# Optimization experiments

Measured on AMD Instinct MI355X. Metric: run time of the kernel, lower is better.

The kernel has to match this reference:

```python
import jax, jax.numpy as jnp
import numpy as np
from jax import lax

B, C, H, W = 8, 64, 128, 128
KS = 3          # kernel size
K = KS * KS     # kernel field = 9
PAD = 1


def conv2d(x, w, b):
    # x: [B,Cin,H,W], w: [Cout,Cin,kh,kw], 'same' 3x3 conv
    y = lax.conv_general_dilated(x, w, window_strides=(1, 1),
                                 padding=((PAD, PAD), (PAD, PAD)),
                                 dimension_numbers=('NCHW', 'OIHW', 'NCHW'))
    return y + b[None, :, None, None]


def modulated_deform_conv(x, offset, mask, weight, bias):
    # x:[B,C,H,W], offset:[B,2K,H,W] (dy,dx per tap), mask:[B,K,H,W]
    Bs, Cin, Hin, Win = x.shape
    off = offset.reshape(Bs, K, 2, Hin, Win)
    ky, kx = jnp.meshgrid(jnp.arange(KS), jnp.arange(KS), indexing='ij')
    ky = ky.reshape(K).astype(x.dtype)   # kernel tap row offsets 0..2
    kx = kx.reshape(K).astype(x.dtype)
    # sampling positions p = p0 + p_k + offset (stride=1, pad=1)
    py = (jnp.arange(Hin, dtype=x.dtype)[None, None, :, None] - PAD
          + ky[None, :, None, None] + off[:, :, 0])            # [B,K,H,W]
    px = (jnp.arange(Win, dtype=x.dtype)[None, None, None, :] - PAD
          + kx[None, :, None, None] + off[:, :, 1])            # [B,K,H,W]

    y0 = jnp.floor(py); x0 = jnp.floor(px)
    ly = py - y0; lx = px - x0                                  # frac parts
    y0i = y0.astype(jnp.int32); x0i = x0.astype(jnp.int32)

    x_flat = x.reshape(Bs, Cin, Hin * Win)

    def gather(iy, ix):
        valid = ((iy >= 0) & (iy < Hin) & (ix >= 0) & (ix < Win))
        flat = (jnp.clip(iy, 0, Hin - 1) * Win + jnp.clip(ix, 0, Win - 1))
        g = jax.vmap(lambda xb, ib: xb[:, ib])(x_flat, flat.reshape(Bs, -1))
        g = g.reshape(Bs, Cin, K, Hin, Win)
        return g * valid[:, None].astype(x.dtype)

    w00 = ((1 - ly) * (1 - lx))[:, None]  # [B,1,K,H,W]
    w01 = ((1 - ly) * lx)[:, None]
    w10 = (ly * (1 - lx))[:, None]
    w11 = (ly * lx)[:, None]

    val = (w00 * gather(y0i, x0i) + w01 * gather(y0i, x0i + 1)
           + w10 * gather(y0i + 1, x0i) + w11 * gather(y0i + 1, x0i + 1))
    val = val * mask[:, None]                                   # modulation
    out = jnp.einsum('ock,bckhw->bohw', weight.reshape(weight.shape[0], Cin, K), val)
    return out + bias[None, :, None, None]


def setup_inputs() -> dict:
    key = jax.random.key(0)
    ks = jax.random.split(key, 7)
    s = 0.05
    return {
        'x': jax.random.normal(ks[0], (B, C, H, W), jnp.float32),
        'w_om': jax.random.normal(ks[1], (3 * K, C, KS, KS), jnp.float32) * s,
        'b_om': jax.random.normal(ks[2], (3 * K,), jnp.float32) * s,
        'w_dc': jax.random.normal(ks[3], (C, C, KS, KS), jnp.float32) * s,
        'b_dc': jax.random.normal(ks[4], (C,), jnp.float32) * s,
        'w_c': jax.random.normal(ks[5], (C, C, KS, KS), jnp.float32) * s,
        'b_c': jax.random.normal(ks[6], (C,), jnp.float32) * s,
    }


def reference(x, w_om, b_om, w_dc, b_dc, w_c, b_c):
    om = conv2d(x, w_om, b_om)                       # [B,3K,H,W]
    offset, mask_raw = om[:, :2 * K], om[:, 2 * K:]
    mask = 2.0 * jax.nn.sigmoid(mask_raw)
    out = modulated_deform_conv(x, offset, mask, w_dc, b_dc)
    act = jnp.where(out > 0, out, 0.2 * out)         # LeakyReLU(0.2)
    return conv2d(act, w_c, b_c) + x
```

## Files before the change

kernel.cpp:

```cpp
#include <hip/hip_runtime.h>
#include <math.h>

#define Bn 8
#define Cn 64
#define Hn 128
#define Wn 128
#define HWn (Hn * Wn)

#define WOM_OFF 0
#define WDC_OFF 18432
#define WC_OFF 55296

typedef __attribute__((ext_vector_type(8))) short short8;
typedef __attribute__((ext_vector_type(4))) float floatx4;

__device__ __forceinline__ float bf2f(short s) {
  return __uint_as_float(((unsigned)(unsigned short)s) << 16);
}
__device__ __forceinline__ short f2bf(float f) {
  unsigned u = __float_as_uint(f);
  u += 0x7fff + ((u >> 16) & 1);
  return (short)(u >> 16);
}

__global__ __launch_bounds__(256) void k_prep_w(
    const float* __restrict__ w_om, const float* __restrict__ w_dc,
    const float* __restrict__ w_c, short* __restrict__ wt) {
  int idx = blockIdx.x * 256 + threadIdx.x;
  if (idx >= 92160) return;
  float v;
  if (idx < WDC_OFF) {
    int e = idx;
    int elem = e & 7, lane = (e >> 3) & 63, mt = (e >> 9) & 1, t = e >> 10;
    int kk = t % 9, cc = t / 9;
    int row = mt * 16 + (lane & 15);
    int cin = cc * 32 + (lane >> 4) * 8 + elem;
    v = (row < 27) ? w_om[(row * 64 + cin) * 9 + kk] : 0.f;
  } else {
    int e = (idx < WC_OFF) ? idx - WDC_OFF : idx - WC_OFF;
    const float* src = (idx < WC_OFF) ? w_dc : w_c;
    int elem = e & 7, lane = (e >> 3) & 63, mt = (e >> 9) & 3, t = e >> 11;
    int kk = t % 9, cc = t / 9;
    int row = mt * 16 + (lane & 15);
    int cin = cc * 32 + (lane >> 4) * 8 + elem;
    v = src[(row * 64 + cin) * 9 + kk];
  }
  wt[idx] = f2bf(v);
}

__global__ __launch_bounds__(256) void k_prep_x(const float* __restrict__ x,
                                                short* __restrict__ xT) {
  __shared__ float tile[64][129];
  const int bid = blockIdx.x;
  const int b = bid & 7, h = bid >> 3;
  const int tid = threadIdx.x;
  const float* xb = x + (size_t)b * 64 * HWn + h * Wn;
  for (int i = tid; i < 8192; i += 256) {
    int c = i >> 7, w = i & 127;
    tile[c][w] = xb[c * HWn + w];
  }
  __syncthreads();
  short* dst = xT + ((size_t)(b * Hn + h) * Wn) * 64;
  for (int i = tid; i < 2048; i += 256) {
    int w = i >> 4, c4 = (i & 15) * 4;
    short4 o;
    o.x = f2bf(tile[c4 + 0][w]);
    o.y = f2bf(tile[c4 + 1][w]);
    o.z = f2bf(tile[c4 + 2][w]);
    o.w = f2bf(tile[c4 + 3][w]);
    *(short4*)(dst + (size_t)w * 64 + c4) = o;
  }
}

__global__ __launch_bounds__(512, 4) void k_omdef(
    const short* __restrict__ xT, const short* __restrict__ wt,
    const float* __restrict__ b_om, const float* __restrict__ b_dc,
    short* __restrict__ actT) {
  __shared__ float som[27 * 132];

  const int bid = blockIdx.x;
  const int b = bid & 7;
  const int h = bid >> 3;
  const int tid = threadIdx.x;
  const int wave = tid >> 6, lane = tid & 63, quad = lane >> 4, lr = lane & 15;
  const short* xb = xT + (size_t)b * HWn * 64;
  const int pxl = wave * 16 + lr;

  floatx4 zf = {0.f, 0.f, 0.f, 0.f};
  const short8 zz = (short8){0, 0, 0, 0, 0, 0, 0, 0};

  floatx4 aco[2] = {zf, zf};
#pragma unroll 3
  for (int kk = 0; kk < 9; ++kk) {
    int ky = kk / 3, kx = kk - ky * 3;
    int gy = h + ky - 1, gx = pxl + kx - 1;
    bool ok = ((unsigned)gy < (unsigned)Hn) && ((unsigned)gx < (unsigned)Wn);
    int gyc = min(max(gy, 0), Hn - 1), gxc = min(max(gx, 0), Wn - 1);
    const short* rec = xb + (size_t)(gyc * Wn + gxc) * 64 + quad * 8;
#pragma unroll
    for (int cc = 0; cc < 2; ++cc) {
      short8 bf = *(const short8*)(rec + cc * 32);
      if (!ok) bf = zz;
      short8 a0 = *(const short8*)(wt + WOM_OFF +
                                   ((cc * 9 + kk) * 2 + 0) * 512 + lane * 8);
      short8 a1 = *(const short8*)(wt + WOM_OFF +
                                   ((cc * 9 + kk) * 2 + 1) * 512 + lane * 8);
      aco[0] = __builtin_amdgcn_mfma_f32_16x16x32_bf16(a0, bf, aco[0], 0, 0, 0);
      aco[1] = __builtin_amdgcn_mfma_f32_16x16x32_bf16(a1, bf, aco[1], 0, 0, 0);
    }
  }
#pragma unroll
  for (int mt = 0; mt < 2; ++mt) {
#pragma unroll
    for (int rr = 0; rr < 4; ++rr) {
      int co = mt * 16 + quad * 4 + rr;
      if (co < 27) {
        float v = aco[mt][rr] + b_om[co];
        if (co >= 18) v = 2.f / (1.f + expf(-v));
        som[co * 132 + pxl] = v;
      }
    }
  }
  asm volatile("s_waitcnt lgkmcnt(0)" ::: "memory");

  floatx4 acc[4] = {zf, zf, zf, zf};
  const short* wdc = wt + WDC_OFF;
  const int cq = quad * 8;
#pragma unroll 3
  for (int kk = 0; kk < 9; ++kk) {
    float offy = som[(2 * kk) * 132 + pxl];
    float offx = som[(2 * kk + 1) * 132 + pxl];
    float m = som[(18 + kk) * 132 + pxl];
    float py = (float)(h - 1 + (kk / 3)) + offy;
    float px_ = (float)(pxl - 1 + (kk % 3)) + offx;
    float fy = floorf(py), fx = floorf(px_);
    float ly = py - fy, lx = px_ - fx;
    int iy0 = (int)fy, ix0 = (int)fx;
    int iy1 = iy0 + 1, ix1 = ix0 + 1;
    bool vy0 = ((unsigned)iy0 < (unsigned)Hn);
    bool vy1 = ((unsigned)iy1 < (unsigned)Hn);
    bool vx0 = ((unsigned)ix0 < (unsigned)Wn);
    bool vx1 = ((unsigned)ix1 < (unsigned)Wn);
    unsigned cy0 = (unsigned)min(max(iy0, 0), Hn - 1);
    unsigned cy1 = (unsigned)min(max(iy1, 0), Hn - 1);
    unsigned cx0 = (unsigned)min(max(ix0, 0), Wn - 1);
    unsigned cx1 = (unsigned)min(max(ix1, 0), Wn - 1);
    unsigned d0 = cy0 * Wn + cx0, d1 = cy0 * Wn + cx1;
    unsigned d2 = cy1 * Wn + cx0, d3 = cy1 * Wn + cx1;
    float u0 = (vy0 && vx0) ? (1.f - ly) * (1.f - lx) * m : 0.f;
    float u1 = (vy0 && vx1) ? (1.f - ly) * lx * m : 0.f;
    float u2 = (vy1 && vx0) ? ly * (1.f - lx) * m : 0.f;
    float u3 = (vy1 && vx1) ? ly * lx * m : 0.f;

    short8 q0 = *(const short8*)(xb + (size_t)d0 * 64 + cq);
    short8 q1 = *(const short8*)(xb + (size_t)d1 * 64 + cq);
    short8 q2 = *(const short8*)(xb + (size_t)d2 * 64 + cq);
    short8 q3 = *(const short8*)(xb + (size_t)d3 * 64 + cq);
    short8 r0 = *(const short8*)(xb + (size_t)d0 * 64 + 32 + cq);
    short8 r1 = *(const short8*)(xb + (size_t)d1 * 64 + 32 + cq);
    short8 r2 = *(const short8*)(xb + (size_t)d2 * 64 + 32 + cq);
    short8 r3 = *(const short8*)(xb + (size_t)d3 * 64 + 32 + cq);

    short8 bf0, bf1;
#pragma unroll
    for (int e = 0; e < 8; ++e) {
      float f = u0 * bf2f(q0[e]) + u1 * bf2f(q1[e]) + u2 * bf2f(q2[e]) +
                u3 * bf2f(q3[e]);
      bf0[e] = f2bf(f);
    }
#pragma unroll
    for (int e = 0; e < 8; ++e) {
      float f = u0 * bf2f(r0[e]) + u1 * bf2f(r1[e]) + u2 * bf2f(r2[e]) +
                u3 * bf2f(r3[e]);
      bf1[e] = f2bf(f);
    }

#pragma unroll
    for (int mt = 0; mt < 4; ++mt) {
      short8 a0 = *(const short8*)(wdc + ((0 * 9 + kk) * 4 + mt) * 512 +
                                   lane * 8);
      acc[mt] = __builtin_amdgcn_mfma_f32_16x16x32_bf16(a0, bf0, acc[mt], 0, 0, 0);
    }
#pragma unroll
    for (int mt = 0; mt < 4; ++mt) {
      short8 a1 = *(const short8*)(wdc + ((1 * 9 + kk) * 4 + mt) * 512 +
                                   lane * 8);
      acc[mt] = __builtin_amdgcn_mfma_f32_16x16x32_bf16(a1, bf1, acc[mt], 0, 0, 0);
    }
  }

  short* ab = actT + ((size_t)(b * Hn + h) * Wn) * 64;
#pragma unroll
  for (int mt = 0; mt < 4; ++mt) {
    int c0 = mt * 16 + quad * 4;
    short4 o;
    float v;
    v = acc[mt][0] + b_dc[c0 + 0]; o.x = f2bf(v > 0.f ? v : 0.2f * v);
    v = acc[mt][1] + b_dc[c0 + 1]; o.y = f2bf(v > 0.f ? v : 0.2f * v);
    v = acc[mt][2] + b_dc[c0 + 2]; o.z = f2bf(v > 0.f ? v : 0.2f * v);
    v = acc[mt][3] + b_dc[c0 + 3]; o.w = f2bf(v > 0.f ? v : 0.2f * v);
    *(short4*)(ab + (size_t)pxl * 64 + c0) = o;
  }
}

__global__ __launch_bounds__(512, 4) void k_conv_out(
    const short* __restrict__ actT, const short* __restrict__ wt,
    const float* __restrict__ b_c, const float* __restrict__ x,
    float* __restrict__ out) {
  __shared__ __attribute__((aligned(16))) short rows[24576];

  const int bid = blockIdx.x;
  const int b = bid & 7;
  const int h = bid >> 3;
  const int tid = threadIdx.x;
  const int wave = tid >> 6, lane = tid & 63, quad = lane >> 4, lr = lane & 15;
  const short* ab = actT + (size_t)b * HWn * 64;
  const int pxl = wave * 16 + lr;

  floatx4 zf = {0.f, 0.f, 0.f, 0.f};
  const short8 zz = (short8){0, 0, 0, 0, 0, 0, 0, 0};
  floatx4 acc[4] = {zf, zf, zf, zf};
  short8* rows8 = (short8*)rows;

  {
    const short8* ar8 = (const short8*)ab;
    for (int i = tid; i < 3072; i += 512) {
      int rr = i >> 10, c = i & 1023;
      int px = c >> 3, sl = c & 7;
      int gy = min(max(h - 1 + rr, 0), Hn - 1);
      short8 v = ar8[(size_t)(gy * Wn + px) * 8 + sl];
      rows8[(rr << 10) + (px << 3) + (sl ^ (px & 7))] = v;
    }
  }
  __syncthreads();

#pragma unroll
  for (int cc = 0; cc < 2; ++cc) {
#pragma unroll
    for (int kk = 0; kk < 9; ++kk) {
      int ky = kk / 3, kx = kk - ky * 3;
      int gy = h + ky - 1, gxx = pxl + kx - 1;
      bool ok = ((unsigned)gy < (unsigned)Hn) && ((unsigned)gxx < (unsigned)Wn);
      int gxc = min(max(gxx, 0), Wn - 1);
      short8 bf = rows8[(ky << 10) + (gxc << 3) + ((cc * 4 + quad) ^ (gxc & 7))];
      if (!ok) bf = zz;
#pragma unroll
      for (int mt = 0; mt < 4; ++mt) {
        short8 am = *(const short8*)(wt + WC_OFF + cc * 18432 +
                                     (kk * 4 + mt) * 512 + lane * 8);
        acc[mt] = __builtin_amdgcn_mfma_f32_16x16x32_bf16(am, bf, acc[mt], 0, 0, 0);
      }
    }
  }
  __syncthreads();

  float* ot = (float*)rows;
#pragma unroll
  for (int mt = 0; mt < 4; ++mt) {
#pragma unroll
    for (int rr = 0; rr < 4; ++rr) {
      ot[(mt * 16 + quad * 4 + rr) * 132 + pxl] = acc[mt][rr];
    }
  }
  __syncthreads();

  const int row = tid >> 3, seg = tid & 7;
  const float bias = b_c[row];
  const size_t gbase = ((size_t)(b * 64 + row) * Hn + h) * Wn + seg * 16;
  const float* xr = x + gbase;
  float* op = out + gbase;
#pragma unroll
  for (int j = 0; j < 4; ++j) {
    floatx4 t = *(const floatx4*)&ot[row * 132 + seg * 16 + j * 4];
    floatx4 xv = *(const floatx4*)&xr[j * 4];
    t = t + xv;
    t[0] += bias; t[1] += bias; t[2] += bias; t[3] += bias;
    *(floatx4*)&op[j * 4] = t;
  }
}

extern "C" void kernel_launch(void* const* d_in, const int* in_sizes, int n_in,
                              void* d_out, int out_size, void* d_ws,
                              size_t ws_size, hipStream_t stream) {
  const float* x = (const float*)d_in[0];
  const float* w_om = (const float*)d_in[1];
  const float* b_om = (const float*)d_in[2];
  const float* w_dc = (const float*)d_in[3];
  const float* b_dc = (const float*)d_in[4];
  const float* w_c = (const float*)d_in[5];
  const float* b_c = (const float*)d_in[6];
  float* out = (float*)d_out;

  short* xT = (short*)d_ws;
  short* actT = xT + (size_t)Bn * HWn * 64;
  short* wt = actT + (size_t)Bn * HWn * 64;

  k_prep_w<<<dim3(360), 256, 0, stream>>>(w_om, w_dc, w_c, wt);
  k_prep_x<<<dim3(1024), 256, 0, stream>>>(x, xT);
  k_omdef<<<dim3(1024), 512, 0, stream>>>(xT, wt, b_om, b_dc, actT);
  k_conv_out<<<dim3(1024), 512, 0, stream>>>(actT, wt, b_c, x, out);
}
```

Baseline: 235.4 us.

## Stage five input rows in swizzled LDS for offset conv and deformable gather

```diff
diff --git a/kernel.cpp b/kernel.cpp
--- a/kernel.cpp
+++ b/kernel.cpp
@@ -72,10 +72,11 @@
   }
 }
 
-__global__ __launch_bounds__(512, 4) void k_omdef(
+__global__ __launch_bounds__(512, 2) void k_omdef(
     const short* __restrict__ xT, const short* __restrict__ wt,
     const float* __restrict__ b_om, const float* __restrict__ b_dc,
     short* __restrict__ actT) {
+  __shared__ __attribute__((aligned(16))) short rows[40960];
   __shared__ float som[27 * 132];
 
   const int bid = blockIdx.x;
@@ -88,6 +89,19 @@
 
   floatx4 zf = {0.f, 0.f, 0.f, 0.f};
   const short8 zz = (short8){0, 0, 0, 0, 0, 0, 0, 0};
+  short8* rows8 = (short8*)rows;
+
+  {
+    const short8* xr8 = (const short8*)xb;
+    for (int i = tid; i < 5120; i += 512) {
+      int rr = i >> 10, c = i & 1023;
+      int px = c >> 3, sl = c & 7;
+      int gy = min(max(h - 2 + rr, 0), Hn - 1);
+      short8 v = xr8[(size_t)(gy * Wn + px) * 8 + sl];
+      rows8[(rr << 10) + (px << 3) + (sl ^ (px & 7))] = v;
+    }
+  }
+  __syncthreads();
 
   floatx4 aco[2] = {zf, zf};
 #pragma unroll 3
@@ -95,11 +109,11 @@
     int ky = kk / 3, kx = kk - ky * 3;
     int gy = h + ky - 1, gx = pxl + kx - 1;
     bool ok = ((unsigned)gy < (unsigned)Hn) && ((unsigned)gx < (unsigned)Wn);
-    int gyc = min(max(gy, 0), Hn - 1), gxc = min(max(gx, 0), Wn - 1);
-    const short* rec = xb + (size_t)(gyc * Wn + gxc) * 64 + quad * 8;
+    int gxc = min(max(gx, 0), Wn - 1);
 #pragma unroll
     for (int cc = 0; cc < 2; ++cc) {
-      short8 bf = *(const short8*)(rec + cc * 32);
+      short8 bf =
+          rows8[((ky + 1) << 10) + (gxc << 3) + ((cc * 4 + quad) ^ (gxc & 7))];
       if (!ok) bf = zz;
       short8 a0 = *(const short8*)(wt + WOM_OFF +
                                    ((cc * 9 + kk) * 2 + 0) * 512 + lane * 8);
@@ -141,25 +155,40 @@
     bool vy1 = ((unsigned)iy1 < (unsigned)Hn);
     bool vx0 = ((unsigned)ix0 < (unsigned)Wn);
     bool vx1 = ((unsigned)ix1 < (unsigned)Wn);
-    unsigned cy0 = (unsigned)min(max(iy0, 0), Hn - 1);
-    unsigned cy1 = (unsigned)min(max(iy1, 0), Hn - 1);
-    unsigned cx0 = (unsigned)min(max(ix0, 0), Wn - 1);
-    unsigned cx1 = (unsigned)min(max(ix1, 0), Wn - 1);
-    unsigned d0 = cy0 * Wn + cx0, d1 = cy0 * Wn + cx1;
-    unsigned d2 = cy1 * Wn + cx0, d3 = cy1 * Wn + cx1;
+    int cy0 = min(max(iy0, 0), Hn - 1);
+    int cy1 = min(max(iy1, 0), Hn - 1);
+    int cx0 = min(max(ix0, 0), Wn - 1);
+    int cx1 = min(max(ix1, 0), Wn - 1);
     float u0 = (vy0 && vx0) ? (1.f - ly) * (1.f - lx) * m : 0.f;
     float u1 = (vy0 && vx1) ? (1.f - ly) * lx * m : 0.f;
     float u2 = (vy1 && vx0) ? ly * (1.f - lx) * m : 0.f;
     float u3 = (vy1 && vx1) ? ly * lx * m : 0.f;
 
-    short8 q0 = *(const short8*)(xb + (size_t)d0 * 64 + cq);
-    short8 q1 = *(const short8*)(xb + (size_t)d1 * 64 + cq);
-    short8 q2 = *(const short8*)(xb + (size_t)d2 * 64 + cq);
-    short8 q3 = *(const short8*)(xb + (size_t)d3 * 64 + cq);
-    short8 r0 = *(const short8*)(xb + (size_t)d0 * 64 + 32 + cq);
-    short8 r1 = *(const short8*)(xb + (size_t)d1 * 64 + 32 + cq);
-    short8 r2 = *(const short8*)(xb + (size_t)d2 * 64 + 32 + cq);
-    short8 r3 = *(const short8*)(xb + (size_t)d3 * 64 + 32 + cq);
+    short8 q0, q1, q2, q3, r0, r1, r2, r3;
+    bool inb = (offy >= -1.0f) && (offy < 1.0f);
+    if (__all((int)inb)) {
+      int j0 = cy0 - h + 2, j1 = cy1 - h + 2;
+      int s0q = (cq >> 3), s1q = 4 + (cq >> 3);
+      q0 = rows8[(j0 << 10) + (cx0 << 3) + (s0q ^ (cx0 & 7))];
+      q1 = rows8[(j0 << 10) + (cx1 << 3) + (s0q ^ (cx1 & 7))];
+      q2 = rows8[(j1 << 10) + (cx0 << 3) + (s0q ^ (cx0 & 7))];
+      q3 = rows8[(j1 << 10) + (cx1 << 3) + (s0q ^ (cx1 & 7))];
+      r0 = rows8[(j0 << 10) + (cx0 << 3) + (s1q ^ (cx0 & 7))];
+      r1 = rows8[(j0 << 10) + (cx1 << 3) + (s1q ^ (cx1 & 7))];
+      r2 = rows8[(j1 << 10) + (cx0 << 3) + (s1q ^ (cx0 & 7))];
+      r3 = rows8[(j1 << 10) + (cx1 << 3) + (s1q ^ (cx1 & 7))];
+    } else {
+      unsigned d0 = (unsigned)(cy0 * Wn + cx0), d1 = (unsigned)(cy0 * Wn + cx1);
+      unsigned d2 = (unsigned)(cy1 * Wn + cx0), d3 = (unsigned)(cy1 * Wn + cx1);
+      q0 = *(const short8*)(xb + (size_t)d0 * 64 + cq);
+      q1 = *(const short8*)(xb + (size_t)d1 * 64 + cq);
+      q2 = *(const short8*)(xb + (size_t)d2 * 64 + cq);
+      q3 = *(const short8*)(xb + (size_t)d3 * 64 + cq);
+      r0 = *(const short8*)(xb + (size_t)d0 * 64 + 32 + cq);
+      r1 = *(const short8*)(xb + (size_t)d1 * 64 + 32 + cq);
+      r2 = *(const short8*)(xb + (size_t)d2 * 64 + 32 + cq);
+      r3 = *(const short8*)(xb + (size_t)d3 * 64 + 32 + cq);
+    }
 
     short8 bf0, bf1;
 #pragma unroll
```

After: 237.2 us. About the same (+0.8%).

## Process two output rows per block and stage weights in LDS

Applied to the files above, without the earlier changes.

```diff
diff --git a/kernel.cpp b/kernel.cpp
--- a/kernel.cpp
+++ b/kernel.cpp
@@ -76,11 +76,12 @@
     const short* __restrict__ xT, const short* __restrict__ wt,
     const float* __restrict__ b_om, const float* __restrict__ b_dc,
     short* __restrict__ actT) {
-  __shared__ float som[27 * 132];
+  __shared__ __attribute__((aligned(16))) short lw[18432];
+  __shared__ float som[2][27 * 132];
 
   const int bid = blockIdx.x;
   const int b = bid & 7;
-  const int h = bid >> 3;
+  const int h0 = (bid >> 3) * 2;
   const int tid = threadIdx.x;
   const int wave = tid >> 6, lane = tid & 63, quad = lane >> 4, lr = lane & 15;
   const short* xb = xT + (size_t)b * HWn * 64;
@@ -89,117 +90,130 @@
   floatx4 zf = {0.f, 0.f, 0.f, 0.f};
   const short8 zz = (short8){0, 0, 0, 0, 0, 0, 0, 0};
 
-  floatx4 aco[2] = {zf, zf};
+  {
+    const short8* src = (const short8*)(wt + WOM_OFF);
+    short8* dst = (short8*)lw;
+    for (int i = tid; i < 2304; i += 512) dst[i] = src[i];
+  }
+  __syncthreads();
+
+  floatx4 aco[2][2] = {{zf, zf}, {zf, zf}};
 #pragma unroll 3
   for (int kk = 0; kk < 9; ++kk) {
     int ky = kk / 3, kx = kk - ky * 3;
-    int gy = h + ky - 1, gx = pxl + kx - 1;
-    bool ok = ((unsigned)gy < (unsigned)Hn) && ((unsigned)gx < (unsigned)Wn);
-    int gyc = min(max(gy, 0), Hn - 1), gxc = min(max(gx, 0), Wn - 1);
-    const short* rec = xb + (size_t)(gyc * Wn + gxc) * 64 + quad * 8;
+    int gx = pxl + kx - 1;
+    bool okx = ((unsigned)gx < (unsigned)Wn);
+    int gxc = min(max(gx, 0), Wn - 1);
 #pragma unroll
     for (int cc = 0; cc < 2; ++cc) {
-      short8 bf = *(const short8*)(rec + cc * 32);
-      if (!ok) bf = zz;
-      short8 a0 = *(const short8*)(wt + WOM_OFF +
-                                   ((cc * 9 + kk) * 2 + 0) * 512 + lane * 8);
-      short8 a1 = *(const short8*)(wt + WOM_OFF +
-                                   ((cc * 9 + kk) * 2 + 1) * 512 + lane * 8);
-      aco[0] = __builtin_amdgcn_mfma_f32_16x16x32_bf16(a0, bf, aco[0], 0, 0, 0);
-      aco[1] = __builtin_amdgcn_mfma_f32_16x16x32_bf16(a1, bf, aco[1], 0, 0, 0);
-    }
-  }
-#pragma unroll
-  for (int mt = 0; mt < 2; ++mt) {
-#pragma unroll
-    for (int rr = 0; rr < 4; ++rr) {
-      int co = mt * 16 + quad * 4 + rr;
-      if (co < 27) {
-        float v = aco[mt][rr] + b_om[co];
-        if (co >= 18) v = 2.f / (1.f + expf(-v));
-        som[co * 132 + pxl] = v;
+      short8 a0 = *(const short8*)&lw[((cc * 9 + kk) * 2 + 0) * 512 + lane * 8];
+      short8 a1 = *(const short8*)&lw[((cc * 9 + kk) * 2 + 1) * 512 + lane * 8];
+#pragma unroll
+      for (int r = 0; r < 2; ++r) {
+        int gy = h0 + r + ky - 1;
+        bool ok = okx && ((unsigned)gy < (unsigned)Hn);
+        int gyc = min(max(gy, 0), Hn - 1);
+        short8 bf = *(const short8*)(xb + (size_t)(gyc * Wn + gxc) * 64 +
+                                     cc * 32 + quad * 8);
+        if (!ok) bf = zz;
+        aco[r][0] = __builtin_amdgcn_mfma_f32_16x16x32_bf16(a0, bf, aco[r][0], 0, 0, 0);
+        aco[r][1] = __builtin_amdgcn_mfma_f32_16x16x32_bf16(a1, bf, aco[r][1], 0, 0, 0);
+      }
+    }
+  }
+#pragma unroll
+  for (int r = 0; r < 2; ++r) {
+#pragma unroll
+    for (int mt = 0; mt < 2; ++mt) {
+#pragma unroll
+      for (int rr = 0; rr < 4; ++rr) {
+        int co = mt * 16 + quad * 4 + rr;
+        if (co < 27) {
+          float v = aco[r][mt][rr] + b_om[co];
+          if (co >= 18) v = 2.f / (1.f + expf(-v));
+          som[r][co * 132 + pxl] = v;
+        }
       }
     }
   }
   asm volatile("s_waitcnt lgkmcnt(0)" ::: "memory");
 
-  floatx4 acc[4] = {zf, zf, zf, zf};
-  const short* wdc = wt + WDC_OFF;
-  const int cq = quad * 8;
+  floatx4 acc[2][4] = {{zf, zf, zf, zf}, {zf, zf, zf, zf}};
+  for (int cc = 0; cc < 2; ++cc) {
+    __syncthreads();
+    {
+      const short8* src = (const short8*)(wt + WDC_OFF + cc * 18432);
+      short8* dst = (short8*)lw;
+      for (int i = tid; i < 2304; i += 512) dst[i] = src[i];
+    }
+    __syncthreads();
+    const int co = cc * 32 + quad * 8;
 #pragma unroll 3
-  for (int kk = 0; kk < 9; ++kk) {
-    float offy = som[(2 * kk) * 132 + pxl];
-    float offx = som[(2 * kk + 1) * 132 + pxl];
-    float m = som[(18 + kk) * 132 + pxl];
-    float py = (float)(h - 1 + (kk / 3)) + offy;
-    float px_ = (float)(pxl - 1 + (kk % 3)) + offx;
-    float fy = floorf(py), fx = floorf(px_);
-    float ly = py - fy, lx = px_ - fx;
-    int iy0 = (int)fy, ix0 = (int)fx;
-    int iy1 = iy0 + 1, ix1 = ix0 + 1;
-    bool vy0 = ((unsigned)iy0 < (unsigned)Hn);
-    bool vy1 = ((unsigned)iy1 < (unsigned)Hn);
-    bool vx0 = ((unsigned)ix0 < (unsigned)Wn);
-    bool vx1 = ((unsigned)ix1 < (unsigned)Wn);
-    unsigned cy0 = (unsigned)min(max(iy0, 0), Hn - 1);
-    unsigned cy1 = (unsigned)min(max(iy1, 0), Hn - 1);
-    unsigned cx0 = (unsigned)min(max(ix0, 0), Wn - 1);
-    unsigned cx1 = (unsigned)min(max(ix1, 0), Wn - 1);
-    unsigned d0 = cy0 * Wn + cx0, d1 = cy0 * Wn + cx1;
-    unsigned d2 = cy1 * Wn + cx0, d3 = cy1 * Wn + cx1;
-    float u0 = (vy0 && vx0) ? (1.f - ly) * (1.f - lx) * m : 0.f;
-    float u1 = (vy0 && vx1) ? (1.f - ly) * lx * m : 0.f;
-    float u2 = (vy1 && vx0) ? ly * (1.f - lx) * m : 0.f;
-    float u3 = (vy1 && vx1) ? ly * lx * m : 0.f;
-
-    short8 q0 = *(const short8*)(xb + (size_t)d0 * 64 + cq);
-    short8 q1 = *(const short8*)(xb + (size_t)d1 * 64 + cq);
-    short8 q2 = *(const short8*)(xb + (size_t)d2 * 64 + cq);
-    short8 q3 = *(const short8*)(xb + (size_t)d3 * 64 + cq);
-    short8 r0 = *(const short8*)(xb + (size_t)d0 * 64 + 32 + cq);
-    short8 r1 = *(const short8*)(xb + (size_t)d1 * 64 + 32 + cq);
-    short8 r2 = *(const short8*)(xb + (size_t)d2 * 64 + 32 + cq);
-    short8 r3 = *(const short8*)(xb + (size_t)d3 * 64 + 32 + cq);
-
-    short8 bf0, bf1;
-#pragma unroll
-    for (int e = 0; e < 8; ++e) {
-      float f = u0 * bf2f(q0[e]) + u1 * bf2f(q1[e]) + u2 * bf2f(q2[e]) +
-                u3 * bf2f(q3[e]);
-      bf0[e] = f2bf(f);
-    }
-#pragma unroll
-    for (int e = 0; e < 8; ++e) {
-      float f = u0 * bf2f(r0[e]) + u1 * bf2f(r1[e]) + u2 * bf2f(r2[e]) +
-                u3 * bf2f(r3[e]);
-      bf1[e] = f2bf(f);
-    }
-
+    for (int kk = 0; kk < 9; ++kk) {
+      short8 am0 = *(const short8*)&lw[(kk * 4 + 0) * 512 + lane * 8];
+      short8 am1 = *(const short8*)&lw[(kk * 4 + 1) * 512 + lane * 8];
+      short8 am2 = *(const short8*)&lw[(kk * 4 + 2) * 512 + lane * 8];
+      short8 am3 = *(const short8*)&lw[(kk * 4 + 3) * 512 + lane * 8];
+#pragma unroll
+      for (int r = 0; r < 2; ++r) {
+        float offy = som[r][(2 * kk) * 132 + pxl];
+        float offx = som[r][(2 * kk + 1) * 132 + pxl];
+        float m = som[r][(18 + kk) * 132 + pxl];
+        float py = (float)(h0 + r - 1 + (kk / 3)) + offy;
+        float px_ = (float)(pxl - 1 + (kk % 3)) + offx;
+        float fy = floorf(py), fx = floorf(px_);
+        float ly = py - fy, lx = px_ - fx;
+        int iy0 = (int)fy, ix0 = (int)fx;
+        int iy1 = iy0 + 1, ix1 = ix0 + 1;
+        bool vy0 = ((unsigned)iy0 < (unsigned)Hn);
+        bool vy1 = ((unsigned)iy1 < (unsigned)Hn);
+        bool vx0 = ((unsigned)ix0 < (unsigned)Wn);
+        bool vx1 = ((unsigned)ix1 < (unsigned)Wn);
+        unsigned cy0 = (unsigned)min(max(iy0, 0), Hn - 1);
+        unsigned cy1 = (unsigned)min(max(iy1, 0), Hn - 1);
+        unsigned cx0 = (unsigned)min(max(ix0, 0), Wn - 1);
+        unsigned cx1 = (unsigned)min(max(ix1, 0), Wn - 1);
+        unsigned d0 = cy0 * Wn + cx0, d1 = cy0 * Wn + cx1;
+        unsigned d2 = cy1 * Wn + cx0, d3 = cy1 * Wn + cx1;
+        float u0 = (vy0 && vx0) ? (1.f - ly) * (1.f - lx) * m : 0.f;
+        float u1 = (vy0 && vx1) ? (1.f - ly) * lx * m : 0.f;
+        float u2 = (vy1 && vx0) ? ly * (1.f - lx) * m : 0.f;
+        float u3 = (vy1 && vx1) ? ly * lx * m : 0.f;
+
+        short8 q0 = *(const short8*)(xb + (size_t)d0 * 64 + co);
+        short8 q1 = *(const short8*)(xb + (size_t)d1 * 64 + co);
+        short8 q2 = *(const short8*)(xb + (size_t)d2 * 64 + co);
+        short8 q3 = *(const short8*)(xb + (size_t)d3 * 64 + co);
+
+        short8 bf;
+#pragma unroll
+        for (int e = 0; e < 8; ++e) {
+          float f = u0 * bf2f(q0[e]) + u1 * bf2f(q1[e]) + u2 * bf2f(q2[e]) +
+                    u3 * bf2f(q3[e]);
+          bf[e] = f2bf(f);
+        }
+        acc[r][0] = __builtin_amdgcn_mfma_f32_16x16x32_bf16(am0, bf, acc[r][0], 0, 0, 0);
+        acc[r][1] = __builtin_amdgcn_mfma_f32_16x16x32_bf16(am1, bf, acc[r][1], 0, 0, 0);
+        acc[r][2] = __builtin_amdgcn_mfma_f32_16x16x32_bf16(am2, bf, acc[r][2], 0, 0, 0);
+        acc[r][3] = __builtin_amdgcn_mfma_f32_16x16x32_bf16(am3, bf, acc[r][3], 0, 0, 0);
+      }
+    }
+  }
+
+#pragma unroll
+  for (int r = 0; r < 2; ++r) {
+    short* ab = actT + ((size_t)(b * Hn + h0 + r) * Wn) * 64;
 #pragma unroll
     for (int mt = 0; mt < 4; ++mt) {
-      short8 a0 = *(const short8*)(wdc + ((0 * 9 + kk) * 4 + mt) * 512 +
-                                   lane * 8);
-      acc[mt] = __builtin_amdgcn_mfma_f32_16x16x32_bf16(a0, bf0, acc[mt], 0, 0, 0);
-    }
-#pragma unroll
-    for (int mt = 0; mt < 4; ++mt) {
-      short8 a1 = *(const short8*)(wdc + ((1 * 9 + kk) * 4 + mt) * 512 +
-                                   lane * 8);
-      acc[mt] = __builtin_amdgcn_mfma_f32_16x16x32_bf16(a1, bf1, acc[mt], 0, 0, 0);
-    }
-  }
-
-  short* ab = actT + ((size_t)(b * Hn + h) * Wn) * 64;
-#pragma unroll
-  for (int mt = 0; mt < 4; ++mt) {
-    int c0 = mt * 16 + quad * 4;
-    short4 o;
-    float v;
-    v = acc[mt][0] + b_dc[c0 + 0]; o.x = f2bf(v > 0.f ? v : 0.2f * v);
-    v = acc[mt][1] + b_dc[c0 + 1]; o.y = f2bf(v > 0.f ? v : 0.2f * v);
-    v = acc[mt][2] + b_dc[c0 + 2]; o.z = f2bf(v > 0.f ? v : 0.2f * v);
-    v = acc[mt][3] + b_dc[c0 + 3]; o.w = f2bf(v > 0.f ? v : 0.2f * v);
-    *(short4*)(ab + (size_t)pxl * 64 + c0) = o;
+      int c0 = mt * 16 + quad * 4;
+      short4 o;
+      float v;
+      v = acc[r][mt][0] + b_dc[c0 + 0]; o.x = f2bf(v > 0.f ? v : 0.2f * v);
+      v = acc[r][mt][1] + b_dc[c0 + 1]; o.y = f2bf(v > 0.f ? v : 0.2f * v);
+      v = acc[r][mt][2] + b_dc[c0 + 2]; o.z = f2bf(v > 0.f ? v : 0.2f * v);
+      v = acc[r][mt][3] + b_dc[c0 + 3]; o.w = f2bf(v > 0.f ? v : 0.2f * v);
+      *(short4*)(ab + (size_t)pxl * 64 + c0) = o;
+    }
   }
 }
 
@@ -207,11 +221,11 @@
     const short* __restrict__ actT, const short* __restrict__ wt,
     const float* __restrict__ b_c, const float* __restrict__ x,
     float* __restrict__ out) {
-  __shared__ __attribute__((aligned(16))) short rows[24576];
+  __shared__ __attribute__((aligned(16))) short lw[18432];
 
   const int bid = blockIdx.x;
   const int b = bid & 7;
-  const int h = bid >> 3;
+  const int h0 = (bid >> 3) * 2;
   const int tid = threadIdx.x;
   const int wave = tid >> 6, lane = tid & 63, quad = lane >> 4, lr = lane & 15;
   const short* ab = actT + (size_t)b * HWn * 64;
@@ -219,63 +233,69 @@
 
   floatx4 zf = {0.f, 0.f, 0.f, 0.f};
   const short8 zz = (short8){0, 0, 0, 0, 0, 0, 0, 0};
-  floatx4 acc[4] = {zf, zf, zf, zf};
-  short8* rows8 = (short8*)rows;
-
-  {
-    const short8* ar8 = (const short8*)ab;
-    for (int i = tid; i < 3072; i += 512) {
-      int rr = i >> 10, c = i & 1023;
-      int px = c >> 3, sl = c & 7;
-      int gy = min(max(h - 1 + rr, 0), Hn - 1);
-      short8 v = ar8[(size_t)(gy * Wn + px) * 8 + sl];
-      rows8[(rr << 10) + (px << 3) + (sl ^ (px & 7))] = v;
-    }
-  }
-  __syncthreads();
-
-#pragma unroll
+  floatx4 acc[2][4] = {{zf, zf, zf, zf}, {zf, zf, zf, zf}};
+
   for (int cc = 0; cc < 2; ++cc) {
-#pragma unroll
+    if (cc) __syncthreads();
+    {
+      const short8* src = (const short8*)(wt + WC_OFF + cc * 18432);
+      short8* dst = (short8*)lw;
+      for (int i = tid; i < 2304; i += 512) dst[i] = src[i];
+    }
+    __syncthreads();
+    const int co = cc * 32 + quad * 8;
+#pragma unroll 3
     for (int kk = 0; kk < 9; ++kk) {
       int ky = kk / 3, kx = kk - ky * 3;
-      int gy = h + ky - 1, gxx = pxl + kx - 1;
-      bool ok = ((unsigned)gy < (unsigned)Hn) && ((unsigned)gxx < (unsigned)Wn);
-      int gxc = min(max(gxx, 0), Wn - 1);
-      short8 bf = rows8[(ky << 10) + (gxc << 3) + ((cc * 4 + quad) ^ (gxc & 7))];
-      if (!ok) bf = zz;
-#pragma unroll
-      for (int mt = 0; mt < 4; ++mt) {
-        short8 am = *(const short8*)(wt + WC_OFF + cc * 18432 +
-                                     (kk * 4 + mt) * 512 + lane * 8);
-        acc[mt] = __builtin_amdgcn_mfma_f32_16x16x32_bf16(am, bf, acc[mt], 0, 0, 0);
+      int gx = pxl + kx - 1;
+      bool okx = ((unsigned)gx < (unsigned)Wn);
+      int gxc = min(max(gx, 0), Wn - 1);
+      short8 am0 = *(const short8*)&lw[(kk * 4 + 0) * 512 + lane * 8];
+      short8 am1 = *(const short8*)&lw[(kk * 4 + 1) * 512 + lane * 8];
+      short8 am2 = *(const short8*)&lw[(kk * 4 + 2) * 512 + lane * 8];
+      short8 am3 = *(const short8*)&lw[(kk * 4 + 3) * 512 + lane * 8];
+#pragma unroll
+      for (int r = 0; r < 2; ++r) {
+        int gy = h0 + r + ky - 1;
+        bool ok = okx && ((unsigned)gy < (unsigned)Hn);
+        int gyc = min(max(gy, 0), Hn - 1);
+        short8 bf = *(const short8*)(ab + (size_t)(gyc * Wn + gxc) * 64 + co);
+        if (!ok) bf = zz;
+        acc[r][0] = __builtin_amdgcn_mfma_f32_16x16x32_bf16(am0, bf, acc[r][0], 0, 0, 0);
+        acc[r][1] = __builtin_amdgcn_mfma_f32_16x16x32_bf16(am1, bf, acc[r][1], 0, 0, 0);
+        acc[r][2] = __builtin_amdgcn_mfma_f32_16x16x32_bf16(am2, bf, acc[r][2], 0, 0, 0);
+        acc[r][3] = __builtin_amdgcn_mfma_f32_16x16x32_bf16(am3, bf, acc[r][3], 0, 0, 0);
       }
     }
   }
   __syncthreads();
 
-  float* ot = (float*)rows;
-#pragma unroll
-  for (int mt = 0; mt < 4; ++mt) {
-#pragma unroll
-    for (int rr = 0; rr < 4; ++rr) {
-      ot[(mt * 16 + quad * 4 + rr) * 132 + pxl] = acc[mt][rr];
-    }
-  }
-  __syncthreads();
-
-  const int row = tid >> 3, seg = tid & 7;
-  const float bias = b_c[row];
-  const size_t gbase = ((size_t)(b * 64 + row) * Hn + h) * Wn + seg * 16;
-  const float* xr = x + gbase;
-  float* op = out + gbase;
-#pragma unroll
-  for (int j = 0; j < 4; ++j) {
-    floatx4 t = *(const floatx4*)&ot[row * 132 + seg * 16 + j * 4];
-    floatx4 xv = *(const floatx4*)&xr[j * 4];
-    t = t + xv;
-    t[0] += bias; t[1] += bias; t[2] += bias; t[3] += bias;
-    *(floatx4*)&op[j * 4] = t;
+  float* ot = (float*)lw;
+#pragma unroll
+  for (int r = 0; r < 2; ++r) {
+    if (r) __syncthreads();
+#pragma unroll
+    for (int mt = 0; mt < 4; ++mt) {
+#pragma unroll
+      for (int rr = 0; rr < 4; ++rr) {
+        ot[(mt * 16 + quad * 4 + rr) * 132 + pxl] = acc[r][mt][rr];
+      }
+    }
+    __syncthreads();
+    const int row = tid >> 3, seg = tid & 7;
+    const float bias = b_c[row];
+    const size_t gbase =
+        ((size_t)(b * 64 + row) * Hn + h0 + r) * Wn + seg * 16;
+    const float* xr = x + gbase;
+    float* op = out + gbase;
+#pragma unroll
+    for (int j = 0; j < 4; ++j) {
+      floatx4 t = *(const floatx4*)&ot[row * 132 + seg * 16 + j * 4];
+      floatx4 xv = *(const floatx4*)&xr[j * 4];
+      t = t + xv;
+      t[0] += bias; t[1] += bias; t[2] += bias; t[3] += bias;
+      *(floatx4*)&op[j * 4] = t;
+    }
   }
 }
 
@@ -297,6 +317,6 @@
 
   k_prep_w<<<dim3(360), 256, 0, stream>>>(w_om, w_dc, w_c, wt);
   k_prep_x<<<dim3(1024), 256, 0, stream>>>(x, xT);
-  k_omdef<<<dim3(1024), 512, 0, stream>>>(xT, wt, b_om, b_dc, actT);
-  k_conv_out<<<dim3(1024), 512, 0, stream>>>(actT, wt, b_c, x, out);
-}
+  k_omdef<<<dim3(512), 512, 0, stream>>>(xT, wt, b_om, b_dc, actT);
+  k_conv_out<<<dim3(512), 512, 0, stream>>>(actT, wt, b_c, x, out);
+}
```

Measured after the change: 217.5 us, median of 2. 7.6% less time.
